# Optimization experiments

Measured on AMD Instinct MI355X. Metric: run time of the kernel, lower is better.

Reference implementation:

```python
import jax, jax.numpy as jnp
import numpy as np
import math

T, P, ITERS, H = 6, 8, 2, 8          # nr_types, num_proto, iters, n_head
D, F = 512, 1024                      # dim_proto, feature_dim (hidden_dim==D)
L = T * ITERS                         # 12 cross-attention layers


def _ln(x, g=None, b=None, eps=1e-5):
    m = x.mean(-1, keepdims=True)
    v = x.var(-1, keepdims=True)
    y = (x - m) * jax.lax.rsqrt(v + eps)
    if g is not None:
        y = y * g + b
    return y


def _forward(x_batch, batch_mask, node_type, pm_W, pm_b, pm_g, pm_bn,
             proto_logsigma, rand_mul, Wq, bq, Wk, bk, Wv, bv, Wo, bo,
             ag, ab, Wm1, bm1, lg, lb, Wm2, bm2, pg, pb):
    B, N, _ = x_batch.shape
    dt = x_batch.dtype
    bm = batch_mask.astype(dt)                                   # [B,N]
    onehot = jax.nn.one_hot(node_type, T, dtype=dt)              # [B,N,T]
    valid = bm * jnp.any(x_batch != 0, axis=-1).astype(dt)       # [B,N]
    mbt = onehot * valid[:, :, None]                             # [B,N,T]
    sums = jnp.einsum('bnt,bnf->btf', mbt, x_batch)              # per-(batch,type) sum
    cnt = mbt.sum(1)                                             # [B,T]
    fallback = x_batch.sum(1) / bm.sum(1, keepdims=True)         # [B,F]
    proto_mu = jnp.where(cnt[..., None] > 0,
                         sums / jnp.maximum(cnt, 1.0)[..., None],
                         fallback[:, None, :])                   # [B,T,F]

    # proto_mlp: Linear + LayerNorm + GELU (dropout = eval/identity)
    mu = jax.nn.gelu(_ln(proto_mu @ pm_W + pm_b, pm_g, pm_bn), approximate=False)  # [B,T,D]
    all_proto = mu[:, :, None, :] + jnp.exp(proto_logsigma)[None] * rand_mul[None]  # [B,T,P,D]

    dh = D // H
    scale = 1.0 / math.sqrt(dh)
    keymask = bm[:, None, None, :] == 0                          # [B,1,1,N]

    def layer(q, i):
        resid = q                                                 # [B,P,D]
        k = _ln((x_batch @ Wk[i] + bk[i]).reshape(B, N, H, dh))   # QK-LayerNorm (no affine)
        v = (x_batch @ Wv[i] + bv[i]).reshape(B, N, H, dh)
        qh = _ln((q @ Wq[i] + bq[i]).reshape(B, P, H, dh))
        dots = jnp.einsum('bkhd,bnhd->bkhn', qh, k) * scale       # [B,P,H,N]
        dots = jnp.where(keymask, -jnp.inf, dots)
        attn = jax.nn.softmax(dots, axis=-1)
        upd = jnp.einsum('bnhd,bkhn->bkhd', v, attn).reshape(B, P, D)
        upd = upd @ Wo[i] + bo[i]
        q = resid + _ln(upd, ag[i], ab[i])
        h = jax.nn.gelu(_ln(q @ Wm1[i] + bm1[i], lg[i], lb[i]), approximate=False)
        h = h @ Wm2[i] + bm2[i]
        return q + _ln(h, pg[i], pb[i])

    outs = []
    c = 0
    for i in range(T):
        p = all_proto[:, i]
        for _ in range(ITERS):
            p = layer(p, c)
            c += 1
        outs.append(p)
    prototypes = jnp.stack(outs, axis=1)                          # [B,T,P,D]
    return prototypes, proto_mu


def setup_inputs() -> dict:
    key = jax.random.key(0)
    ks = jax.random.split(key, 40)
    B, N = 4, 4096
    sc = 0.02

    def rn(i, shape, s=sc):
        return jax.random.normal(ks[i], shape, jnp.float32) * s

    inp = {
        'x_batch': jax.random.normal(ks[0], (B, N, F), jnp.float32),
        'batch_mask': jax.random.randint(ks[1], (B, N), 0, 2, jnp.int32),
        'node_type': jax.random.randint(ks[2], (B, N), 0, T, jnp.int32),
        'pm_W': rn(3, (F, D)), 'pm_b': jnp.zeros((D,)),
        'pm_g': jnp.ones((D,)), 'pm_bn': jnp.zeros((D,)),
        'proto_logsigma': rn(4, (T, 1, D), 0.05),
        'rand_mul': jax.random.normal(ks[5], (T, P, D), jnp.float32),
        'Wq': rn(6, (L, D, D)), 'bq': jnp.zeros((L, D)),
        'Wk': rn(7, (L, F, D)), 'bk': jnp.zeros((L, D)),
        'Wv': rn(8, (L, F, D)), 'bv': jnp.zeros((L, D)),
        'Wo': rn(9, (L, D, D)), 'bo': jnp.zeros((L, D)),
        'ag': jnp.ones((L, D)), 'ab': jnp.zeros((L, D)),
        'Wm1': rn(10, (L, D, D)), 'bm1': jnp.zeros((L, D)),
        'lg': jnp.ones((L, D)), 'lb': jnp.zeros((L, D)),
        'Wm2': rn(11, (L, D, D)), 'bm2': jnp.zeros((L, D)),
        'pg': jnp.ones((L, D)), 'pb': jnp.zeros((L, D)),
    }
    return inp


def reference(x_batch, batch_mask, node_type, pm_W, pm_b, pm_g, pm_bn,
              proto_logsigma, rand_mul, Wq, bq, Wk, bk, Wv, bv, Wo, bo,
              ag, ab, Wm1, bm1, lg, lb, Wm2, bm2, pg, pb):
    return _forward(x_batch, batch_mask, node_type, pm_W, pm_b, pm_g, pm_bn,
                    proto_logsigma, rand_mul, Wq, bq, Wk, bk, Wv, bv, Wo, bo,
                    ag, ab, Wm1, bm1, lg, lb, Wm2, bm2, pg, pb)
```

## Files before the change

### kernel.cpp

```cpp
#include <hip/hip_runtime.h>
#include <hip/hip_bf16.h>
#include <stdint.h>

#define TT 6
#define PP 8
#define HH 8
#define DD 512
#define FF 1024
#define DH 64
#define NB 4
#define NN 4096
#define LL 12
#define NCH 16
#define CHK 256
#define NXB 128

typedef __attribute__((ext_vector_type(8))) short short8v;
typedef __attribute__((ext_vector_type(4))) float f32x4;
typedef __attribute__((ext_vector_type(4))) unsigned short u16x4;
typedef __attribute__((ext_vector_type(8))) unsigned short u16x8;
typedef unsigned short u16;

__device__ __forceinline__ float bf2f(u16 u){
  union { unsigned int i; float f; } x; x.i = ((unsigned int)u) << 16; return x.f;
}
__device__ __forceinline__ u16 f2bf(float f){
  union { float f; unsigned int i; } x; x.f = f;
  unsigned int r = x.i + 0x7fffu + ((x.i >> 16) & 1u);
  return (u16)(r >> 16);
}
__device__ __forceinline__ float wave_sum(float x){
  #pragma unroll
  for (int o = 32; o > 0; o >>= 1) x += __shfl_xor(x, o);
  return x;
}
__device__ __forceinline__ float ldf(const void* p, size_t i, int f32){
  float v;
  if (f32) v = ((const float*)p)[i];
  else     v = bf2f(((const u16*)p)[i]);
  return v;
}
__device__ __forceinline__ float gemv_vec(const float* __restrict__ xs,
    const void* __restrict__ W, size_t wbase, int ktot, int wf32,
    float* __restrict__ red, int tid){
  int g = tid & 63, sl = tid >> 6;
  int kpw = ktot >> 3;
  float a[8] = {0,0,0,0,0,0,0,0};
  if (wf32){
    const float* Wp = (const float*)W + wbase + (size_t)(sl*kpw)*DD + g*8;
    #pragma unroll 4
    for (int i = 0; i < kpw; ++i){
      float xv = xs[sl*kpw + i];
      f32x4 lo = *(const f32x4*)(Wp + (size_t)i*DD);
      f32x4 hi = *(const f32x4*)(Wp + (size_t)i*DD + 4);
      a[0]+=xv*lo.x; a[1]+=xv*lo.y; a[2]+=xv*lo.z; a[3]+=xv*lo.w;
      a[4]+=xv*hi.x; a[5]+=xv*hi.y; a[6]+=xv*hi.z; a[7]+=xv*hi.w;
    }
  } else {
    const u16* Wp = (const u16*)W + wbase + (size_t)(sl*kpw)*DD + g*8;
    #pragma unroll 4
    for (int i = 0; i < kpw; ++i){
      float xv = xs[sl*kpw + i];
      u16x8 w8 = *(const u16x8*)(Wp + (size_t)i*DD);
      #pragma unroll
      for (int j = 0; j < 8; ++j) a[j] += xv * bf2f(w8[j]);
    }
  }
  #pragma unroll
  for (int j = 0; j < 8; ++j) red[sl*512 + g*8 + j] = a[j];
  __syncthreads();
  float y = 0;
  #pragma unroll
  for (int s2 = 0; s2 < 8; ++s2) y += red[s2*512 + tid];
  return y;
}
__device__ __forceinline__ void glds16(const void* g, void* l){
#if __has_builtin(__builtin_amdgcn_global_load_lds)
  __builtin_amdgcn_global_load_lds(
      (const __attribute__((address_space(1))) void*)g,
      (__attribute__((address_space(3))) void*)l, 16, 0, 0);
#else
  *(u16x8*)l = *(const u16x8*)g;
#endif
}
__device__ __forceinline__ void tail_gemm8(f32x4 acc[4], const u16* __restrict__ Bp,
    const u16* As, int l15, int q4, int n0w){
  #pragma unroll
  for (int ni = 0; ni < 4; ++ni){ f32x4 z = {0,0,0,0}; acc[ni] = z; }
  #pragma unroll 2
  for (int k0 = 0; k0 < 512; k0 += 32){
    short8v bf[4], af;
    #pragma unroll
    for (int ni = 0; ni < 4; ++ni)
      bf[ni] = *(const short8v*)(Bp + (size_t)(n0w + ni*16 + l15)*DD + k0 + q4*8);
    af = *(const short8v*)(As + l15*520 + k0 + q4*8);
    #pragma unroll
    for (int ni = 0; ni < 4; ++ni)
      acc[ni] = __builtin_amdgcn_mfma_f32_16x16x32_bf16(af, bf[ni], acc[ni], 0, 0, 0);
  }
}
__device__ __forceinline__ void row_ln8(const f32x4 acc[4],
    float* red1, float* red2, int w, int l15, int q4,
    float mv[4], float rv[4]){
  float s1[4], s2[4];
  #pragma unroll
  for (int r = 0; r < 4; ++r){
    float a0=acc[0][r], a1=acc[1][r], a2=acc[2][r], a3=acc[3][r];
    s1[r] = (a0+a1)+(a2+a3);
    s2[r] = (a0*a0+a1*a1)+(a2*a2+a3*a3);
  }
  #pragma unroll
  for (int o = 1; o < 16; o <<= 1)
    #pragma unroll
    for (int r = 0; r < 4; ++r){
      s1[r] += __shfl_xor(s1[r], o);
      s2[r] += __shfl_xor(s2[r], o);
    }
  if (l15 == 0){
    #pragma unroll
    for (int r = 0; r < 4; ++r){
      int row = q4*4 + r;
      red1[row*8 + w] = s1[r];
      red2[row*8 + w] = s2[r];
    }
  }
  __syncthreads();
  #pragma unroll
  for (int r = 0; r < 4; ++r){
    int row = q4*4 + r;
    float S1 = 0, S2 = 0;
    #pragma unroll
    for (int j = 0; j < 8; ++j){ S1 += red1[row*8+j]; S2 += red2[row*8+j]; }
    float m = S1 * (1.f/DD);
    float var = S2 * (1.f/DD) - m*m;
    mv[r] = m;
    rv[r] = rsqrtf(var + 1e-5f);
  }
  __syncthreads();
}

__global__ void k_detect(const void* __restrict__ X, int* __restrict__ flag){
  int tid = threadIdx.x;
  const u16* u = (const u16*)X;
  int bad = 0;
  for (int i = tid; i < 8192; i += 256){
    int ex = (u[i] >> 7) & 0xFF;
    if (ex >= 0x90) bad = 1;
  }
  __shared__ int s;
  if (tid == 0) s = 0;
  __syncthreads();
  if (bad) s = 1;
  __syncthreads();
  if (tid == 0) *flag = s;
}

__global__ void k_cvt2(const void* __restrict__ s0, u16* __restrict__ d0, int n0q,
                       const void* __restrict__ s1, u16* __restrict__ d1,
                       const int* __restrict__ flagp){
  int f32 = *flagp;
  size_t q = (size_t)blockIdx.x*256 + threadIdx.x;
  const void* s; u16* d; size_t i;
  if (q < (size_t)n0q){ s = s0; d = d0; i = q*4; }
  else                { s = s1; d = d1; i = (q - n0q)*4; }
  if (f32){
    f32x4 v = *(const f32x4*)((const float*)s + i);
    u16x4 o; o.x=f2bf(v.x); o.y=f2bf(v.y); o.z=f2bf(v.z); o.w=f2bf(v.w);
    *(u16x4*)(d+i) = o;
  } else {
    *(u16x4*)(d+i) = *(const u16x4*)((const u16*)s + i);
  }
}

__global__ void k_xcv(const void* __restrict__ X, u16* __restrict__ Xb,
                      const int* __restrict__ bm, const int* __restrict__ ntype,
                      float* __restrict__ Pcol, float* __restrict__ Ptot,
                      float* __restrict__ cnt, float* __restrict__ bmsum,
                      const int* __restrict__ flagp){
  int f32 = *flagp;
  int b = blockIdx.y, blk = blockIdx.x;
  int n0 = blk * 32;
  int tid = threadIdx.x;
  int f0 = tid * 4;
  __shared__ int sflag[32];
  __shared__ float scnt[TT+1];
  if (tid < 32) sflag[tid] = 0;
  if (tid < TT+1) scnt[tid] = 0.f;
  __syncthreads();
  float acc[TT][4] = {};
  float tot[4] = {0,0,0,0};
  for (int i = 0; i < 32; ++i){
    int n = n0 + i;
    size_t idx = (size_t)(b*NN+n)*FF + f0;
    u16x4 xb;
    bool a;
    if (f32){
      f32x4 v = *(const f32x4*)((const float*)X + idx);
      xb.x=f2bf(v.x); xb.y=f2bf(v.y); xb.z=f2bf(v.z); xb.w=f2bf(v.w);
      a = (v.x!=0.f)||(v.y!=0.f)||(v.z!=0.f)||(v.w!=0.f);
    } else {
      xb = *(const u16x4*)((const u16*)X + idx);
      a = (bf2f(xb.x)!=0.f)||(bf2f(xb.y)!=0.f)||(bf2f(xb.z)!=0.f)||(bf2f(xb.w)!=0.f);
    }
    *(u16x4*)(Xb+idx) = xb;
    if (a) sflag[i] = 1;
    float vbm = (bm[b*NN+n] != 0) ? 1.f : 0.f;
    int ty = ntype[b*NN+n];
    #pragma unroll
    for (int j = 0; j < 4; ++j){
      float xv = bf2f(xb[j]);
      tot[j] += xv;
      float xvv = xv * vbm;
      #pragma unroll
      for (int t = 0; t < TT; ++t) acc[t][j] += (ty==t) ? xvv : 0.f;
    }
  }
  __syncthreads();
  if (tid < 32){
    int n = n0 + tid;
    if (bm[b*NN+n] != 0){
      if (sflag[tid]) atomicAdd(&scnt[ntype[b*NN+n]], 1.f);
      atomicAdd(&scnt[TT], 1.f);
    }
  }
  size_t pbase = (size_t)blk*NB + b;
  #pragma unroll
  for (int t = 0; t < TT; ++t){
    f32x4 v = {acc[t][0], acc[t][1], acc[t][2], acc[t][3]};
    *(f32x4*)&Pcol[(pbase*TT + t)*FF + f0] = v;
  }
  {
    f32x4 v = {tot[0], tot[1], tot[2], tot[3]};
    *(f32x4*)&Ptot[pbase*FF + f0] = v;
  }
  __syncthreads();
  if (tid < TT) atomicAdd(&cnt[b*TT + tid], scnt[tid]);
  if (tid == TT) atomicAdd(&bmsum[b], scnt[TT]);
}

__global__ void k_fold(const float* __restrict__ Pcol, const float* __restrict__ Ptot,
                       float* __restrict__ colsums, float* __restrict__ coltotal){
  int fb = blockIdx.x;
  int bt = blockIdx.y;
  int b = bt / TT, t = bt % TT;
  int f = fb*256 + threadIdx.x;
  float S = 0.f;
  #pragma unroll 4
  for (int blk = 0; blk < NXB; ++blk)
    S += Pcol[(((size_t)blk*NB + b)*TT + t)*FF + f];
  colsums[(size_t)bt*FF + f] = S;
  if (t == 0){
    float T = 0.f;
    #pragma unroll 4
    for (int blk = 0; blk < NXB; ++blk)
      T += Ptot[((size_t)blk*NB + b)*FF + f];
    coltotal[b*FF + f] = T;
  }
}

__global__ void k_compact(const int* __restrict__ bm, int* __restrict__ nidx,
                          int* __restrict__ cntc){
  int b = blockIdx.x, tid = threadIdx.x;
  __shared__ int csum[256];
  __shared__ int pref[257];
  int base = b*NN + tid*16;
  int f[16]; int loc = 0;
  #pragma unroll
  for (int i = 0; i < 16; ++i){ f[i] = (bm[base+i] != 0); loc += f[i]; }
  csum[tid] = loc;
  __syncthreads();
  if (tid == 0){
    pref[0] = 0;
    for (int j = 0; j < 256; ++j) pref[j+1] = pref[j] + csum[j];
  }
  __syncthreads();
  int off = b*NN + pref[tid];
  #pragma unroll
  for (int i = 0; i < 16; ++i){ if (f[i]) nidx[off++] = tid*16 + i; }
  if (tid == 0) cntc[b] = pref[256];
}

__global__ void k_wbfT(const void* __restrict__ Wq, const void* __restrict__ Wo,
                       const void* __restrict__ Wm1, const void* __restrict__ Wm2,
                       u16* __restrict__ Wt, const int* __restrict__ flagp){
  int f32 = *flagp;
  int z = blockIdx.z;
  int fam = z / LL;
  const void* src = (fam==0) ? Wq : (fam==1) ? Wo : (fam==2) ? Wm1 : Wm2;
  size_t sbase = (size_t)(z % LL) * DD * DD;
  __shared__ u16 tile[32][33];
  int d0 = blockIdx.x*32, k0 = blockIdx.y*32;
  int tx = threadIdx.x, ty = threadIdx.y;
  #pragma unroll
  for (int i = 0; i < 4; ++i){
    size_t idx = sbase + (size_t)(k0 + ty + i*8)*DD + d0 + tx;
    u16 v;
    if (f32) v = f2bf(((const float*)src)[idx]);
    else     v = ((const u16*)src)[idx];
    tile[ty + i*8][tx] = v;
  }
  __syncthreads();
  #pragma unroll
  for (int i = 0; i < 4; ++i)
    Wt[((size_t)z*DD + d0 + ty + i*8)*DD + k0 + tx] = tile[tx][ty + i*8];
}

__global__ void __launch_bounds__(512) k_mu(const float* __restrict__ colsums,
   const float* __restrict__ coltotal, const float* __restrict__ cnt,
   const float* __restrict__ bmsum,
   const void* __restrict__ pmWx, const void* __restrict__ pmb,
   const void* __restrict__ pmg, const void* __restrict__ pmbn,
   const void* __restrict__ lsig, const void* __restrict__ rmul,
   float* __restrict__ qstate, void* __restrict__ dout, int wmode,
   const int* __restrict__ flagp){
  int f32 = *flagp;
  int wf32 = wmode ? f32 : 0;
  const size_t OFFP = (size_t)NB*TT*PP*DD;
  int bt = blockIdx.x; int b = bt/TT, t = bt%TT;
  int d = threadIdx.x;
  __shared__ float xs[FF];
  __shared__ float red[4096];
  __shared__ float r1[8], r2[8];
  float cv = cnt[bt];
  float inv = 1.f / fmaxf(cv, 1.f);
  float fbinv = 1.f / bmsum[b];
  #pragma unroll
  for (int h = 0; h < 2; ++h){
    int f = d + h*512;
    float pm = (cv > 0.f) ? colsums[(size_t)bt*FF + f] * inv
                          : coltotal[b*FF + f] * fbinv;
    xs[f] = pm;
    if (f32) ((float*)dout)[OFFP + (size_t)bt*FF + f] = pm;
    else     ((u16*)dout)[OFFP + (size_t)bt*FF + f] = f2bf(pm);
  }
  __syncthreads();
  float acc = ldf(pmb, d, f32) + gemv_vec(xs, pmWx, 0, FF, wf32, red, d);
  int lane = d & 63, wid = d >> 6;
  float s1 = wave_sum(acc), s2 = wave_sum(acc*acc);
  if (lane==0){ r1[wid]=s1; r2[wid]=s2; }
  __syncthreads();
  float m=0, qq=0;
  #pragma unroll
  for (int i=0;i<8;++i){ m+=r1[i]; qq+=r2[i]; }
  m *= (1.f/DD); float var = qq*(1.f/DD) - m*m;
  float y = (acc - m) * rsqrtf(var + 1e-5f) * ldf(pmg, d, f32) + ldf(pmbn, d, f32);
  float mu = 0.5f * y * (1.f + erff(y * 0.70710678118654752f));
  #pragma unroll
  for (int p = 0; p < PP; ++p){
    float rv = ldf(rmul, (size_t)(t*PP+p)*DD + d, f32);
    float ls = ldf(lsig, (size_t)t*DD + d, f32);
    qstate[(((size_t)(b*TT+t))*PP + p)*DD + d] = mu + expf(ls) * rv;
  }
}

__global__ void k_transpose(const void* __restrict__ Wk, const void* __restrict__ Wv,
                            u16* __restrict__ TK, u16* __restrict__ TV,
                            int tlo, int s, const int* __restrict__ flagp){
  int f32 = *flagp;
  int ti = blockIdx.z >> 1, kv = blockIdx.z & 1;
  int c = 2*(tlo+ti)+s;
  size_t eoff = (size_t)c*FF*DD;
  const void* W = kv ? Wv : Wk;
  u16* T = (kv ? TV : TK) + (size_t)ti*FF*DD;
  __shared__ u16 tile[32][33];
  int n0 = blockIdx.x * 32, k0 = blockIdx.y * 32;
  int tx = threadIdx.x, ty = threadIdx.y;
  #pragma unroll
  for (int i = 0; i < 4; ++i){
    size_t idx = eoff + (size_t)(k0 + ty + i*8)*DD + n0 + tx;
    u16 v;
    if (f32) v = f2bf(((const float*)W)[idx]);
    else     v = ((const u16*)W)[idx];
    tile[ty + i*8][tx] = v;
  }
  __syncthreads();
  #pragma unroll
  for (int i = 0; i < 4; ++i)
    T[(size_t)(n0 + ty + i*8)*FF + k0 + tx] = tile[tx][ty + i*8];
}

__global__ void __launch_bounds__(512) k_kvgemm(const u16* __restrict__ Xb,
    const u16* __restrict__ TK, const u16* __restrict__ TV,
    const void* __restrict__ bk, const void* __restrict__ bv,
    u16* __restrict__ Kb, u16* __restrict__ Vb,
    const int* __restrict__ nidx, const int* __restrict__ cntc,
    int tlo, int s, int nt, const int* __restrict__ flagp){
  int f32 = *flagp;
  int orig = blockIdx.x;
  int x = orig & 7, r = orig >> 3;
  int bx = r / nt, pr = r - bx*nt;
  int pairg = x*nt + pr;
  int by = pairg & 3; int kvti = pairg >> 2; int kv = kvti & 1; int ti = kvti >> 1;
  int b = bx >> 4, jt = bx & 15;
  int cnt = cntc[b];
  if (jt*256 >= cnt) return;
  int c = 2*(tlo+ti)+s;
  size_t boff = (size_t)c*DD;
  const u16* WT = (kv ? TV : TK) + (size_t)ti*FF*DD;
  const void* bias = kv ? bv : bk;
  u16* out = (kv ? Vb : Kb) + (size_t)ti*((size_t)NB*NN*DD);
  int n0 = by*128;
  __shared__ __align__(16) char LDS[3*24576];
  int tid = threadIdx.x, wid = tid >> 6, lane = tid & 63;
  int wr = wid >> 1, wcn = wid & 1;
  const u16* gp0; const u16* gp1; const u16* gp2;
  int lo0, lo1, lo2;
  {
    const u16* gps[3]; int los[3];
    #pragma unroll
    for (int i = 0; i < 3; ++i){
      int e = tid + i*512;
      if (e < 1024){
        int row = e>>2, sp = e&3;
        int ssrc = sp ^ (((row>>3)&1)<<1);
        int cl = jt*256 + row; if (cl >= cnt) cl = cnt-1;
        int grow = nidx[b*NN + cl];
        gps[i] = Xb + ((size_t)b*NN + grow)*FF + ssrc*8;
        los[i] = e*16;
      } else {
        int e2 = e - 1024;
        int row = e2>>2, sp = e2&3;
        int ssrc = sp ^ (((row>>3)&1)<<1);
        gps[i] = WT + (size_t)(n0 + row)*FF + ssrc*8;
        los[i] = 16384 + e2*16;
      }
    }
    gp0=gps[0]; gp1=gps[1]; gp2=gps[2];
    lo0=los[0]; lo1=los[1]; lo2=los[2];
  }
#define STAGE(T) { char* bb_ = LDS + ((T)%3)*24576; \
  glds16(gp0 + (T)*32, bb_ + lo0); glds16(gp1 + (T)*32, bb_ + lo1); \
  glds16(gp2 + (T)*32, bb_ + lo2); }
  int ke = (lane>>4) ^ (((lane>>3)&1)<<1);
  int arow[4], brow[4];
  #pragma unroll
  for (int mi = 0; mi < 4; ++mi)
    arow[mi] = (wr*64 + mi*16 + (lane&15))*64 + ke*16;
  #pragma unroll
  for (int ni = 0; ni < 4; ++ni)
    brow[ni] = 16384 + (wcn*64 + ni*16 + (lane&15))*64 + ke*16;
  f32x4 acc[4][4] = {};
  STAGE(0);
  STAGE(1);
  asm volatile("s_waitcnt vmcnt(3)" ::: "memory");
  __builtin_amdgcn_sched_barrier(0);
  __builtin_amdgcn_s_barrier();
  __builtin_amdgcn_sched_barrier(0);
  #pragma unroll
  for (int t = 0; t < 32; ++t){
    const char* Bbuf = LDS + (t%3)*24576;
    short8v af[4], bf[4];
    #pragma unroll
    for (int mi = 0; mi < 4; ++mi)
      af[mi] = *(const short8v*)(Bbuf + arow[mi]);
    #pragma unroll
    for (int ni = 0; ni < 4; ++ni)
      bf[ni] = *(const short8v*)(Bbuf + brow[ni]);
    if (t + 2 <= 31) STAGE(t+2);
    __builtin_amdgcn_s_setprio(1);
    #pragma unroll
    for (int mi = 0; mi < 4; ++mi)
      #pragma unroll
      for (int ni = 0; ni < 4; ++ni)
        acc[mi][ni] = __builtin_amdgcn_mfma_f32_16x16x32_bf16(af[mi], bf[ni], acc[mi][ni], 0, 0, 0);
    __builtin_amdgcn_s_setprio(0);
    if (t < 30)       asm volatile("s_waitcnt vmcnt(3)" ::: "memory");
    else if (t == 30) asm volatile("s_waitcnt vmcnt(0)" ::: "memory");
    __builtin_amdgcn_sched_barrier(0);
    if (t < 31){
      __builtin_amdgcn_s_barrier();
      __builtin_amdgcn_sched_barrier(0);
    }
  }
#undef STAGE
  #pragma unroll
  for (int mi = 0; mi < 4; ++mi){
    #pragma unroll
    for (int ni = 0; ni < 4; ++ni){
      int col = n0 + wcn*64 + ni*16 + (lane & 15);
      int h = col >> 6, dh = col & 63;
      float bvf = ldf(bias, boff + col, f32);
      #pragma unroll
      for (int r2 = 0; r2 < 4; ++r2){
        int row = jt*256 + wr*64 + mi*16 + (lane>>4)*4 + r2;
        out[(((size_t)(b*HH + h))*NN + row)*DH + dh] = f2bf(acc[mi][ni][r2] + bvf);
      }
    }
  }
}

__global__ void __launch_bounds__(512) k_qproj(const float* __restrict__ qstate,
      const void* __restrict__ Wq, const void* __restrict__ bq,
      float* __restrict__ qh, int tlo, int s, int wmode,
      const int* __restrict__ flagp){
  int f32 = *flagp;
  int wf32 = wmode ? f32 : 0;
  int z = blockIdx.x; int ti = z >> 5, rr = z & 31;
  int b = rr >> 3, p = rr & 7;
  int t = tlo + ti, c = 2*t + s;
  size_t woff = (size_t)c*DD*DD, boff = (size_t)c*DD;
  int d = threadIdx.x;
  __shared__ float xs[DD];
  __shared__ float red[4096];
  const float* xrow = qstate + (((size_t)(b*TT+t))*PP + p)*DD;
  xs[d] = xrow[d];
  __syncthreads();
  float acc = ldf(bq, boff + d, f32) + gemv_vec(xs, Wq, woff, DD, wf32, red, d);
  float s1 = wave_sum(acc) * (1.f/DH);
  float s2 = wave_sum(acc*acc) * (1.f/DH);
  float var = s2 - s1*s1;
  qh[(size_t)z*DD + d] = (acc - s1) * rsqrtf(var + 1e-5f);
}

__global__ void __launch_bounds__(512) k_attnA(const u16* __restrict__ Kb,
     const u16* __restrict__ Vb, const float* __restrict__ qh,
     const int* __restrict__ cntc, float* __restrict__ Opart, float* __restrict__ lpart){
  int ic = blockIdx.x, bh = blockIdx.y, ti = blockIdx.z;
  int b = bh >> 3, h = bh & 7;
  int cnt = cntc[b];
  if (ic*CHK >= cnt) return;
  int tid = threadIdx.x, p8 = tid >> 6, ln = tid & 63;
  int r8 = ln >> 3, g = ln & 7;
  __shared__ __align__(16) char KV[32768];
  __shared__ float qs[PP*DH];
  __shared__ float qsum[PP];
  __shared__ float e_lds[CHK*9];
  int rem = cnt - ic*CHK;
  float qv = qh[((size_t)(ti*32 + b*PP + p8))*DD + h*DH + ln];
  size_t tioff = (size_t)ti*((size_t)NB*NN*DD);
  const u16* Kbase = Kb + tioff + ((size_t)(b*HH + h)*NN + (size_t)ic*CHK)*DH;
  const u16* Vbase = Vb + tioff + ((size_t)(b*HH + h)*NN + (size_t)ic*CHK)*DH;
  #pragma unroll
  for (int i = 0; i < 4; ++i){
    int e = tid + i*512;
    int row = e >> 3, sp = e & 7;
    int ss = sp ^ (row & 7);
    int rr = row < rem ? row : rem-1;
    glds16(Vbase + (size_t)rr*DH + ss*8, (char*)KV + e*16);
  }
  qs[p8*DH + ln] = qv;
  {
    float sQ = wave_sum(qv);
    if (ln == 0) qsum[p8] = sQ;
  }
  asm volatile("s_waitcnt lgkmcnt(0)" ::: "memory");
  __builtin_amdgcn_sched_barrier(0);
  __builtin_amdgcn_s_barrier();
  __builtin_amdgcn_sched_barrier(0);
  #pragma unroll
  for (int it = 0; it < CHK/64; ++it){
    int nl = it*64 + p8*8 + r8;
    int rr8 = nl < rem ? nl : rem-1;
    u16x8 kv8 = *(const u16x8*)(Kbase + (size_t)rr8*DH + g*8);
    float kf[8];
    #pragma unroll
    for (int e = 0; e < 8; ++e) kf[e] = bf2f(kv8[e]);
    float sm = 0, sq = 0;
    #pragma unroll
    for (int e = 0; e < 8; ++e){ sm += kf[e]; sq += kf[e]*kf[e]; }
    #pragma unroll
    for (int o = 1; o < 8; o <<= 1){
      sm += __shfl_xor(sm, o);
      sq += __shfl_xor(sq, o);
    }
    sm *= (1.f/DH); sq = sq*(1.f/DH) - sm*sm;
    float inv = rsqrtf(sq + 1e-5f);
    float ap[8];
    #pragma unroll
    for (int p = 0; p < 8; ++p){
      f32x4 qa = *(const f32x4*)&qs[p*DH + g*8];
      f32x4 qb = *(const f32x4*)&qs[p*DH + g*8 + 4];
      ap[p] = kf[0]*qa.x + kf[1]*qa.y + kf[2]*qa.z + kf[3]*qa.w
            + kf[4]*qb.x + kf[5]*qb.y + kf[6]*qb.z + kf[7]*qb.w;
    }
    #pragma unroll
    for (int o = 1; o < 8; o <<= 1){
      #pragma unroll
      for (int p = 0; p < 8; ++p) ap[p] += __shfl_xor(ap[p], o);
    }
    float dg = (g==0)?ap[0]:(g==1)?ap[1]:(g==2)?ap[2]:(g==3)?ap[3]
             : (g==4)?ap[4]:(g==5)?ap[5]:(g==6)?ap[6]:ap[7];
    float sv = (dg - sm*qsum[g]) * inv * 0.125f;
    e_lds[nl*9 + g] = (nl < rem) ? __expf(sv) : 0.f;
  }
  __syncthreads();
  {
    float lp = 0;
    #pragma unroll
    for (int j = 0; j < CHK/64; ++j) lp += e_lds[(ln + j*64)*9 + p8];
    lp = wave_sum(lp);
    if (ln == 0) lpart[((size_t)(ti*32+bh)*NCH + ic)*PP + p8] = lp;
  }
  {
    float a0=0,a1=0,a2=0,a3=0,a4=0,a5=0,a6=0,a7=0;
    int vseg = (r8 ^ g) * 16;
    #pragma unroll 4
    for (int m = 0; m < CHK/8; ++m){
      float e = e_lds[(g + m*8)*9 + p8];
      u16x8 vv = *(const u16x8*)((const char*)KV + (g + m*8)*128 + vseg);
      a0 += e*bf2f(vv[0]); a1 += e*bf2f(vv[1]);
      a2 += e*bf2f(vv[2]); a3 += e*bf2f(vv[3]);
      a4 += e*bf2f(vv[4]); a5 += e*bf2f(vv[5]);
      a6 += e*bf2f(vv[6]); a7 += e*bf2f(vv[7]);
    }
    #pragma unroll
    for (int o = 1; o < 8; o <<= 1){
      a0 += __shfl_xor(a0, o); a1 += __shfl_xor(a1, o);
      a2 += __shfl_xor(a2, o); a3 += __shfl_xor(a3, o);
      a4 += __shfl_xor(a4, o); a5 += __shfl_xor(a5, o);
      a6 += __shfl_xor(a6, o); a7 += __shfl_xor(a7, o);
    }
    if (g == 0){
      float* op = Opart + ((size_t)(ti*32+bh)*NCH + ic)*512 + p8*64 + r8*8;
      f32x4 lo = {a0,a1,a2,a3}, hi = {a4,a5,a6,a7};
      *(f32x4*)op = lo;
      *((f32x4*)op + 1) = hi;
    }
  }
}

__global__ void __launch_bounds__(512) k_tailm(
    const float* __restrict__ Opart, const float* __restrict__ lpart,
    const int* __restrict__ cntc,
    float* __restrict__ qstate, float* __restrict__ qh,
    const u16* __restrict__ Wt,
    const void* __restrict__ bo, const void* __restrict__ ag, const void* __restrict__ ab,
    const void* __restrict__ bm1, const void* __restrict__ lg, const void* __restrict__ lb,
    const void* __restrict__ bm2, const void* __restrict__ pg, const void* __restrict__ pb,
    const void* __restrict__ bq, void* __restrict__ dout,
    int tlo, int s, int nt, const int* __restrict__ flagp){
  int f32 = *flagp;
  int ti = blockIdx.x & 7, b = blockIdx.x >> 3;
  if (ti >= nt) return;
  int t = tlo + ti, c = 2*t + s;
  int tid = threadIdx.x;
  int w = tid >> 6, lane = tid & 63, q4 = lane >> 4, l15 = lane & 15;
  int n0w = w*64;
  size_t boff = (size_t)c*DD;
  const size_t famSz = (size_t)LL*DD*DD;
  __shared__ u16 As[16*520];
  __shared__ float red1[128], red2[128];
  __shared__ float lval[64];
  int nch = (cntc[b] + CHK - 1) / CHK;
  for (int i = tid; i < 16*520; i += 512) As[i] = 0;
  if (tid < 64){
    int p = tid >> 3, hh = tid & 7;
    float l = 0;
    for (int ic = 0; ic < nch; ++ic)
      l += lpart[((size_t)(ti*32 + b*8 + hh)*NCH + ic)*PP + p];
    lval[tid] = 1.f / l;
  }
  __syncthreads();
  {
    int hh = tid >> 6, dd = tid & 63;
    #pragma unroll
    for (int p = 0; p < 8; ++p){
      float o = 0;
      for (int ic = 0; ic < nch; ++ic)
        o += Opart[((size_t)(ti*32 + b*8 + hh)*NCH + ic)*512 + p*64 + dd];
      As[p*520 + hh*64 + dd] = f2bf(o * lval[p*8 + hh]);
    }
  }
  __syncthreads();
  f32x4 acc[4], q2[4];
  float mv[4], rv[4];
  size_t qoffb = ((size_t)(b*TT+t))*PP*DD;
  {
    const u16* Bp = Wt + famSz + (size_t)c*DD*DD;
    tail_gemm8(acc, Bp, As, l15, q4, n0w);
    #pragma unroll
    for (int ni = 0; ni < 4; ++ni){
      float bv = ldf(bo, boff + n0w + ni*16 + l15, f32);
      #pragma unroll
      for (int r = 0; r < 4; ++r) acc[ni][r] += bv;
    }
    row_ln8(acc, red1, red2, w, l15, q4, mv, rv);
    #pragma unroll
    for (int ni = 0; ni < 4; ++ni){
      int col = n0w + ni*16 + l15;
      float gm = ldf(ag, boff + col, f32), bt = ldf(ab, boff + col, f32);
      #pragma unroll
      for (int r = 0; r < 4; ++r){
        int row = q4*4 + r;
        float y = (acc[ni][r] - mv[r])*rv[r]*gm + bt;
        float res = (q4 < 2) ? qstate[qoffb + (size_t)row*DD + col] : 0.f;
        q2[ni][r] = res + y;
      }
    }
    if (q4 < 2){
      #pragma unroll
      for (int r = 0; r < 4; ++r){
        int row = q4*4 + r;
        #pragma unroll
        for (int ni = 0; ni < 4; ++ni)
          As[row*520 + n0w + ni*16 + l15] = f2bf(q2[ni][r]);
      }
    }
  }
  __syncthreads();
  {
    const u16* Bp = Wt + 2*famSz + (size_t)c*DD*DD;
    tail_gemm8(acc, Bp, As, l15, q4, n0w);
    #pragma unroll
    for (int ni = 0; ni < 4; ++ni){
      float bv = ldf(bm1, boff + n0w + ni*16 + l15, f32);
      #pragma unroll
      for (int r = 0; r < 4; ++r) acc[ni][r] += bv;
    }
    row_ln8(acc, red1, red2, w, l15, q4, mv, rv);
    #pragma unroll
    for (int ni = 0; ni < 4; ++ni){
      int col = n0w + ni*16 + l15;
      float gm = ldf(lg, boff + col, f32), bt = ldf(lb, boff + col, f32);
      #pragma unroll
      for (int r = 0; r < 4; ++r){
        int row = q4*4 + r;
        float y = (acc[ni][r] - mv[r])*rv[r]*gm + bt;
        y = 0.5f*y*(1.f + erff(y*0.70710678118654752f));
        if (q4 < 2) As[row*520 + col] = f2bf(y);
      }
    }
  }
  __syncthreads();
  {
    const u16* Bp = Wt + 3*famSz + (size_t)c*DD*DD;
    tail_gemm8(acc, Bp, As, l15, q4, n0w);
    #pragma unroll
    for (int ni = 0; ni < 4; ++ni){
      float bv = ldf(bm2, boff + n0w + ni*16 + l15, f32);
      #pragma unroll
      for (int r = 0; r < 4; ++r) acc[ni][r] += bv;
    }
    row_ln8(acc, red1, red2, w, l15, q4, mv, rv);
    #pragma unroll
    for (int ni = 0; ni < 4; ++ni){
      int col = n0w + ni*16 + l15;
      float gm = ldf(pg, boff + col, f32), bt = ldf(pb, boff + col, f32);
      #pragma unroll
      for (int r = 0; r < 4; ++r){
        int row = q4*4 + r;
        float outv = q2[ni][r] + (acc[ni][r] - mv[r])*rv[r]*gm + bt;
        if (q4 < 2){
          qstate[qoffb + (size_t)row*DD + col] = outv;
          if (s == 0) As[row*520 + col] = f2bf(outv);
          else {
            if (f32) ((float*)dout)[qoffb + (size_t)row*DD + col] = outv;
            else     ((u16*)dout)[qoffb + (size_t)row*DD + col] = f2bf(outv);
          }
        }
      }
    }
  }
  if (s == 0){
    __syncthreads();
    const u16* Bp = Wt + (size_t)(c+1)*DD*DD;
    tail_gemm8(acc, Bp, As, l15, q4, n0w);
    #pragma unroll
    for (int ni = 0; ni < 4; ++ni){
      float bv = ldf(bq, (size_t)(c+1)*DD + n0w + ni*16 + l15, f32);
      #pragma unroll
      for (int r = 0; r < 4; ++r) acc[ni][r] += bv;
    }
    float s1[4], s2[4];
    #pragma unroll
    for (int r = 0; r < 4; ++r){
      float a0=acc[0][r], a1=acc[1][r], a2=acc[2][r], a3=acc[3][r];
      s1[r] = (a0+a1)+(a2+a3);
      s2[r] = (a0*a0+a1*a1)+(a2*a2+a3*a3);
    }
    #pragma unroll
    for (int o = 1; o < 16; o <<= 1)
      #pragma unroll
      for (int r = 0; r < 4; ++r){
        s1[r] += __shfl_xor(s1[r], o);
        s2[r] += __shfl_xor(s2[r], o);
      }
    if (q4 < 2){
      #pragma unroll
      for (int r = 0; r < 4; ++r){
        int row = q4*4 + r;
        float m = s1[r] * (1.f/DH);
        float var = s2[r] * (1.f/DH) - m*m;
        float ri = rsqrtf(var + 1e-5f);
        #pragma unroll
        for (int ni = 0; ni < 4; ++ni){
          int col = n0w + ni*16 + l15;
          qh[((size_t)(ti*32 + b*8 + row))*DD + col] = (acc[ni][r] - m)*ri;
        }
      }
    }
  }
}

__global__ void __launch_bounds__(512) k_tail(
    const float* __restrict__ Opart, const float* __restrict__ lpart,
    const int* __restrict__ cntc,
    float* __restrict__ qstate, float* __restrict__ qh,
    const void* __restrict__ Wo_, const void* __restrict__ Wm1_,
    const void* __restrict__ Wm2_, const void* __restrict__ Wq_,
    const void* __restrict__ bo, const void* __restrict__ ag, const void* __restrict__ ab,
    const void* __restrict__ bm1, const void* __restrict__ lg, const void* __restrict__ lb,
    const void* __restrict__ bm2, const void* __restrict__ pg, const void* __restrict__ pb,
    const void* __restrict__ bq,
    int tlo, int s, int wmode, const int* __restrict__ flagp){
  int f32 = *flagp;
  int wf32 = wmode ? f32 : 0;
  int z = blockIdx.x; int ti = z >> 5, rr = z & 31;
  int b = rr >> 3, p = rr & 7;
  int t = tlo + ti, c = 2*t + s;
  int d = threadIdx.x;
  int h = d >> 6, dd = d & 63;
  int lane = d & 63, wid = d >> 6;
  size_t qoff = (((size_t)(b*TT+t))*PP + p)*DD;
  size_t boff = (size_t)c*DD;
  size_t w0 = (size_t)c*DD*DD;
  __shared__ float xs[DD];
  __shared__ float red[4096];
  __shared__ float r1[8], r2[8];
  int nch = (cntc[b] + CHK - 1) / CHK;
  float o = 0, l = 0;
  for (int ic = 0; ic < nch; ++ic){
    o += Opart[((size_t)(ti*32 + b*8 + h)*NCH + ic)*512 + p*64 + dd];
    l += lpart[((size_t)(ti*32 + b*8 + h)*NCH + ic)*PP + p];
  }
  float upd = o / l;
  xs[d] = upd;
  __syncthreads();
  float acc = ldf(bo, boff + d, f32) + gemv_vec(xs, Wo_, w0, DD, wf32, red, d);
  {
    float s1 = wave_sum(acc), s2 = wave_sum(acc*acc);
    if (lane == 0){ r1[wid] = s1; r2[wid] = s2; }
  }
  __syncthreads();
  float m = 0, qv = 0;
  #pragma unroll
  for (int i = 0; i < 8; ++i){ m += r1[i]; qv += r2[i]; }
  m *= (1.f/DD); float var = qv*(1.f/DD) - m*m;
  float y = (acc - m)*rsqrtf(var + 1e-5f)*ldf(ag, boff+d, f32) + ldf(ab, boff+d, f32);
  float q2 = qstate[qoff + d] + y;
  __syncthreads();
  xs[d] = q2;
  __syncthreads();
  float acc2 = ldf(bm1, boff + d, f32) + gemv_vec(xs, Wm1_, w0, DD, wf32, red, d);
  {
    float s1 = wave_sum(acc2), s2 = wave_sum(acc2*acc2);
    if (lane == 0){ r1[wid] = s1; r2[wid] = s2; }
  }
  __syncthreads();
  m = 0; qv = 0;
  #pragma unroll
  for (int i = 0; i < 8; ++i){ m += r1[i]; qv += r2[i]; }
  m *= (1.f/DD); var = qv*(1.f/DD) - m*m;
  float y2 = (acc2 - m)*rsqrtf(var + 1e-5f)*ldf(lg, boff+d, f32) + ldf(lb, boff+d, f32);
  y2 = 0.5f*y2*(1.f + erff(y2*0.70710678118654752f));
  __syncthreads();
  xs[d] = y2;
  __syncthreads();
  float acc3 = ldf(bm2, boff + d, f32) + gemv_vec(xs, Wm2_, w0, DD, wf32, red, d);
  {
    float s1 = wave_sum(acc3), s2 = wave_sum(acc3*acc3);
    if (lane == 0){ r1[wid] = s1; r2[wid] = s2; }
  }
  __syncthreads();
  m = 0; qv = 0;
  #pragma unroll
  for (int i = 0; i < 8; ++i){ m += r1[i]; qv += r2[i]; }
  m *= (1.f/DD); var = qv*(1.f/DD) - m*m;
  float y3 = (acc3 - m)*rsqrtf(var + 1e-5f)*ldf(pg, boff+d, f32) + ldf(pb, boff+d, f32);
  float outv = q2 + y3;
  qstate[qoff + d] = outv;
  if (s == 0){
    __syncthreads();
    xs[d] = outv;
    __syncthreads();
    size_t w1 = (size_t)(c+1)*DD*DD;
    float accq = ldf(bq, (size_t)(c+1)*DD + d, f32) + gemv_vec(xs, Wq_, w1, DD, wf32, red, d);
    float t1 = wave_sum(accq) * (1.f/DH);
    float t2 = wave_sum(accq*accq) * (1.f/DH);
    float var2 = t2 - t1*t1;
    qh[(size_t)z*DD + d] = (accq - t1) * rsqrtf(var2 + 1e-5f);
  }
}

__global__ void k_out(const float* __restrict__ qstate, void* __restrict__ dout,
                      const int* __restrict__ flagp){
  int f32 = *flagp;
  int i = blockIdx.x*256 + threadIdx.x;
  if (f32) ((float*)dout)[i] = qstate[i];
  else     ((u16*)dout)[i] = f2bf(qstate[i]);
}

extern "C" void kernel_launch(void* const* d_in, const int* in_sizes, int n_in,
                              void* d_out, int out_size, void* d_ws, size_t ws_size,
                              hipStream_t stream){
  (void)in_sizes; (void)n_in; (void)out_size;
  const void* X   = d_in[0];
  const int* bm    = (const int*)d_in[1];
  const int* ntype = (const int*)d_in[2];
  const void* pmW = d_in[3];  const void* pmb = d_in[4];
  const void* pmg = d_in[5];  const void* pmbn= d_in[6];
  const void* lsig= d_in[7];  const void* rmul= d_in[8];
  const void* Wq  = d_in[9];  const void* bq  = d_in[10];
  const void* Wk  = d_in[11]; const void* bk  = d_in[12];
  const void* Wv  = d_in[13]; const void* bv  = d_in[14];
  const void* Wo  = d_in[15]; const void* bo  = d_in[16];
  const void* ag  = d_in[17]; const void* ab  = d_in[18];
  const void* Wm1 = d_in[19]; const void* bm1 = d_in[20];
  const void* lg  = d_in[21]; const void* lb  = d_in[22];
  const void* Wm2 = d_in[23]; const void* bm2 = d_in[24];
  const void* pg  = d_in[25]; const void* pb  = d_in[26];

  char* ws = (char*)d_ws;
  int*   flagp    = (int*)(ws + 0);
  float* cnt      = (float*)(ws + 256);
  float* bmsum    = (float*)(ws + 512);
  float* colsums  = (float*)(ws + 768);
  float* coltotal = (float*)(ws + 99072);
  float* qstate   = (float*)(ws + 279296);
  int*   cntc     = (int*)(ws + 672512);
  int*   nidx     = (int*)(ws + 672768);

  size_t off = 738304;
  auto take = [&](size_t bytes)->char*{
    char* p = ws + off; off = (off + bytes + 255) & ~(size_t)255; return p;
  };
  u16* Xbf = (u16*)take((size_t)NB*NN*FF*2);

  const size_t perT = (size_t)65536
                    + 16384
                    + 1048576
                    + 2*1048576
                    + 2*16777216;
  const size_t wtBytes = (size_t)4*LL*DD*DD*2;
  const size_t pmwbB   = (size_t)FF*DD*2;
  const size_t wqbB    = (size_t)LL*DD*DD*2;
  size_t base = off;

  int nt = 1;
  if      (ws_size >= base + 6*perT + 65536) nt = 6;
  else if (ws_size >= base + 3*perT + 65536) nt = 3;
  else if (ws_size >= base + 2*perT + 65536) nt = 2;

  float* qh    = (float*)take((size_t)nt*65536);
  float* lpart = (float*)take((size_t)nt*16384);
  float* Opart = (float*)take((size_t)nt*1048576);
  u16*   WkT   = (u16*)take((size_t)nt*1048576);
  u16*   WvT   = (u16*)take((size_t)nt*1048576);
  u16*   Kb    = (u16*)take((size_t)nt*16777216);
  u16*   Vb    = (u16*)take((size_t)nt*16777216);

  int useWt = (ws_size >= off + wtBytes + 65536) ? 1 : 0;
  u16* Wt = useWt ? (u16*)take(wtBytes) : nullptr;
  int useCvt = (ws_size >= off + pmwbB + wqbB + 65536) ? 1 : 0;
  u16* pmWb = useCvt ? (u16*)take(pmwbB) : nullptr;
  u16* Wqb  = useCvt ? (u16*)take(wqbB)  : nullptr;

  const void* WqG = useCvt ? (const void*)Wqb : Wq;
  int wmode = useCvt ? 0 : 1;

  float* Pcol = (float*)Kb;
  float* Ptot = (float*)((char*)Kb + (size_t)NXB*NB*TT*FF*4);

  hipMemsetAsync(ws + 256, 0, 512, stream);
  k_detect<<<1, 256, 0, stream>>>(X, flagp);
  k_compact<<<NB, 256, 0, stream>>>(bm, nidx, cntc);
  if (useWt)
    k_wbfT<<<dim3(16, 16, 4*LL), dim3(32, 8), 0, stream>>>(Wq, Wo, Wm1, Wm2, Wt, flagp);
  if (useCvt){
    const int n0q = (FF*DD)/4;
    const int nblk = (FF*DD + LL*DD*DD)/4/256;
    k_cvt2<<<nblk, 256, 0, stream>>>(pmW, pmWb, n0q, Wq, Wqb, flagp);
  }
  k_xcv<<<dim3(NXB, NB), 256, 0, stream>>>(X, Xbf, bm, ntype, Pcol, Ptot,
                                           cnt, bmsum, flagp);
  k_fold<<<dim3(4, NB*TT), 256, 0, stream>>>(Pcol, Ptot, colsums, coltotal);
  if (useCvt)
    k_mu<<<NB*TT, 512, 0, stream>>>(colsums, coltotal, cnt, bmsum,
        pmWb, pmb, pmg, pmbn, lsig, rmul, qstate, d_out, 0, flagp);
  else
    k_mu<<<NB*TT, 512, 0, stream>>>(colsums, coltotal, cnt, bmsum,
        pmW, pmb, pmg, pmbn, lsig, rmul, qstate, d_out, 1, flagp);

  for (int tlo = 0; tlo < TT; tlo += nt){
    for (int s = 0; s < 2; ++s){
      k_transpose<<<dim3(16, 32, 2*nt), dim3(32, 8), 0, stream>>>(
          Wk, Wv, WkT, WvT, tlo, s, flagp);
      k_kvgemm<<<64*8*nt, 512, 0, stream>>>(
          Xbf, WkT, WvT, bk, bv, Kb, Vb, nidx, cntc, tlo, s, nt, flagp);
      if (s == 0)
        k_qproj<<<nt*32, 512, 0, stream>>>(qstate, WqG, bq, qh, tlo, 0, wmode, flagp);
      k_attnA<<<dim3(NCH, 32, nt), 512, 0, stream>>>(Kb, Vb, qh, cntc, Opart, lpart);
      if (useWt)
        k_tailm<<<32, 512, 0, stream>>>(Opart, lpart, cntc, qstate, qh, Wt,
            bo, ag, ab, bm1, lg, lb, bm2, pg, pb, bq, d_out, tlo, s, nt, flagp);
      else
        k_tail<<<nt*32, 512, 0, stream>>>(Opart, lpart, cntc, qstate, qh,
            Wo, Wm1, Wm2, Wq, bo, ag, ab, bm1, lg, lb, bm2, pg, pb, bq,
            tlo, s, 1, flagp);
    }
  }
  if (!useWt)
    k_out<<<NB*TT*PP*DD/256, 256, 0, stream>>>(qstate, d_out, flagp);
}
```

Measured before the change: 619.0 us.

## Drop MFMA tail kernel and transposed bf16 weight prep; use per-row GEMV tail

Removes the k_wbfT pre-transposition of Wq/Wo/Wm1/Wm2 into bf16 and the k_tailm MFMA tail, which ran only 32 blocks (one per batch×type slot, batched over prototypes). Every launch now uses the per-row k_tail GEMV path over nt*32 blocks, which reads the original weights and, when the converted copy exists, the bf16 Wq. k_tail now writes the final output on the second sub-iteration, so the separate k_out kernel is no longer launched. The aim is to save the upfront weight transpose and spread the tail over more blocks. The cost is scalar GEMV work instead of matrix-core MFMA, and Wo, Wm1 and Wm2 are re-read from the original, possibly fp32, inputs.

```diff
diff --git a/kernel.cpp b/kernel.cpp
--- a/kernel.cpp
+++ b/kernel.cpp
@@ -82,61 +82,6 @@
 #else
   *(u16x8*)l = *(const u16x8*)g;
 #endif
-}
-__device__ __forceinline__ void tail_gemm8(f32x4 acc[4], const u16* __restrict__ Bp,
-    const u16* As, int l15, int q4, int n0w){
-  #pragma unroll
-  for (int ni = 0; ni < 4; ++ni){ f32x4 z = {0,0,0,0}; acc[ni] = z; }
-  #pragma unroll 2
-  for (int k0 = 0; k0 < 512; k0 += 32){
-    short8v bf[4], af;
-    #pragma unroll
-    for (int ni = 0; ni < 4; ++ni)
-      bf[ni] = *(const short8v*)(Bp + (size_t)(n0w + ni*16 + l15)*DD + k0 + q4*8);
-    af = *(const short8v*)(As + l15*520 + k0 + q4*8);
-    #pragma unroll
-    for (int ni = 0; ni < 4; ++ni)
-      acc[ni] = __builtin_amdgcn_mfma_f32_16x16x32_bf16(af, bf[ni], acc[ni], 0, 0, 0);
-  }
-}
-__device__ __forceinline__ void row_ln8(const f32x4 acc[4],
-    float* red1, float* red2, int w, int l15, int q4,
-    float mv[4], float rv[4]){
-  float s1[4], s2[4];
-  #pragma unroll
-  for (int r = 0; r < 4; ++r){
-    float a0=acc[0][r], a1=acc[1][r], a2=acc[2][r], a3=acc[3][r];
-    s1[r] = (a0+a1)+(a2+a3);
-    s2[r] = (a0*a0+a1*a1)+(a2*a2+a3*a3);
-  }
-  #pragma unroll
-  for (int o = 1; o < 16; o <<= 1)
-    #pragma unroll
-    for (int r = 0; r < 4; ++r){
-      s1[r] += __shfl_xor(s1[r], o);
-      s2[r] += __shfl_xor(s2[r], o);
-    }
-  if (l15 == 0){
-    #pragma unroll
-    for (int r = 0; r < 4; ++r){
-      int row = q4*4 + r;
-      red1[row*8 + w] = s1[r];
-      red2[row*8 + w] = s2[r];
-    }
-  }
-  __syncthreads();
-  #pragma unroll
-  for (int r = 0; r < 4; ++r){
-    int row = q4*4 + r;
-    float S1 = 0, S2 = 0;
-    #pragma unroll
-    for (int j = 0; j < 8; ++j){ S1 += red1[row*8+j]; S2 += red2[row*8+j]; }
-    float m = S1 * (1.f/DD);
-    float var = S2 * (1.f/DD) - m*m;
-    mv[r] = m;
-    rv[r] = rsqrtf(var + 1e-5f);
-  }
-  __syncthreads();
 }
 
 __global__ void k_detect(const void* __restrict__ X, int* __restrict__ flag){
@@ -278,31 +223,6 @@
   #pragma unroll
   for (int i = 0; i < 16; ++i){ if (f[i]) nidx[off++] = tid*16 + i; }
   if (tid == 0) cntc[b] = pref[256];
-}
-
-__global__ void k_wbfT(const void* __restrict__ Wq, const void* __restrict__ Wo,
-                       const void* __restrict__ Wm1, const void* __restrict__ Wm2,
-                       u16* __restrict__ Wt, const int* __restrict__ flagp){
-  int f32 = *flagp;
-  int z = blockIdx.z;
-  int fam = z / LL;
-  const void* src = (fam==0) ? Wq : (fam==1) ? Wo : (fam==2) ? Wm1 : Wm2;
-  size_t sbase = (size_t)(z % LL) * DD * DD;
-  __shared__ u16 tile[32][33];
-  int d0 = blockIdx.x*32, k0 = blockIdx.y*32;
-  int tx = threadIdx.x, ty = threadIdx.y;
-  #pragma unroll
-  for (int i = 0; i < 4; ++i){
-    size_t idx = sbase + (size_t)(k0 + ty + i*8)*DD + d0 + tx;
-    u16 v;
-    if (f32) v = f2bf(((const float*)src)[idx]);
-    else     v = ((const u16*)src)[idx];
-    tile[ty + i*8][tx] = v;
-  }
-  __syncthreads();
-  #pragma unroll
-  for (int i = 0; i < 4; ++i)
-    Wt[((size_t)z*DD + d0 + ty + i*8)*DD + k0 + tx] = tile[tx][ty + i*8];
 }
 
 __global__ void __launch_bounds__(512) k_mu(const float* __restrict__ colsums,
@@ -619,179 +539,6 @@
   }
 }
 
-__global__ void __launch_bounds__(512) k_tailm(
-    const float* __restrict__ Opart, const float* __restrict__ lpart,
-    const int* __restrict__ cntc,
-    float* __restrict__ qstate, float* __restrict__ qh,
-    const u16* __restrict__ Wt,
-    const void* __restrict__ bo, const void* __restrict__ ag, const void* __restrict__ ab,
-    const void* __restrict__ bm1, const void* __restrict__ lg, const void* __restrict__ lb,
-    const void* __restrict__ bm2, const void* __restrict__ pg, const void* __restrict__ pb,
-    const void* __restrict__ bq, void* __restrict__ dout,
-    int tlo, int s, int nt, const int* __restrict__ flagp){
-  int f32 = *flagp;
-  int ti = blockIdx.x & 7, b = blockIdx.x >> 3;
-  if (ti >= nt) return;
-  int t = tlo + ti, c = 2*t + s;
-  int tid = threadIdx.x;
-  int w = tid >> 6, lane = tid & 63, q4 = lane >> 4, l15 = lane & 15;
-  int n0w = w*64;
-  size_t boff = (size_t)c*DD;
-  const size_t famSz = (size_t)LL*DD*DD;
-  __shared__ u16 As[16*520];
-  __shared__ float red1[128], red2[128];
-  __shared__ float lval[64];
-  int nch = (cntc[b] + CHK - 1) / CHK;
-  for (int i = tid; i < 16*520; i += 512) As[i] = 0;
-  if (tid < 64){
-    int p = tid >> 3, hh = tid & 7;
-    float l = 0;
-    for (int ic = 0; ic < nch; ++ic)
-      l += lpart[((size_t)(ti*32 + b*8 + hh)*NCH + ic)*PP + p];
-    lval[tid] = 1.f / l;
-  }
-  __syncthreads();
-  {
-    int hh = tid >> 6, dd = tid & 63;
-    #pragma unroll
-    for (int p = 0; p < 8; ++p){
-      float o = 0;
-      for (int ic = 0; ic < nch; ++ic)
-        o += Opart[((size_t)(ti*32 + b*8 + hh)*NCH + ic)*512 + p*64 + dd];
-      As[p*520 + hh*64 + dd] = f2bf(o * lval[p*8 + hh]);
-    }
-  }
-  __syncthreads();
-  f32x4 acc[4], q2[4];
-  float mv[4], rv[4];
-  size_t qoffb = ((size_t)(b*TT+t))*PP*DD;
-  {
-    const u16* Bp = Wt + famSz + (size_t)c*DD*DD;
-    tail_gemm8(acc, Bp, As, l15, q4, n0w);
-    #pragma unroll
-    for (int ni = 0; ni < 4; ++ni){
-      float bv = ldf(bo, boff + n0w + ni*16 + l15, f32);
-      #pragma unroll
-      for (int r = 0; r < 4; ++r) acc[ni][r] += bv;
-    }
-    row_ln8(acc, red1, red2, w, l15, q4, mv, rv);
-    #pragma unroll
-    for (int ni = 0; ni < 4; ++ni){
-      int col = n0w + ni*16 + l15;
-      float gm = ldf(ag, boff + col, f32), bt = ldf(ab, boff + col, f32);
-      #pragma unroll
-      for (int r = 0; r < 4; ++r){
-        int row = q4*4 + r;
-        float y = (acc[ni][r] - mv[r])*rv[r]*gm + bt;
-        float res = (q4 < 2) ? qstate[qoffb + (size_t)row*DD + col] : 0.f;
-        q2[ni][r] = res + y;
-      }
-    }
-    if (q4 < 2){
-      #pragma unroll
-      for (int r = 0; r < 4; ++r){
-        int row = q4*4 + r;
-        #pragma unroll
-        for (int ni = 0; ni < 4; ++ni)
-          As[row*520 + n0w + ni*16 + l15] = f2bf(q2[ni][r]);
-      }
-    }
-  }
-  __syncthreads();
-  {
-    const u16* Bp = Wt + 2*famSz + (size_t)c*DD*DD;
-    tail_gemm8(acc, Bp, As, l15, q4, n0w);
-    #pragma unroll
-    for (int ni = 0; ni < 4; ++ni){
-      float bv = ldf(bm1, boff + n0w + ni*16 + l15, f32);
-      #pragma unroll
-      for (int r = 0; r < 4; ++r) acc[ni][r] += bv;
-    }
-    row_ln8(acc, red1, red2, w, l15, q4, mv, rv);
-    #pragma unroll
-    for (int ni = 0; ni < 4; ++ni){
-      int col = n0w + ni*16 + l15;
-      float gm = ldf(lg, boff + col, f32), bt = ldf(lb, boff + col, f32);
-      #pragma unroll
-      for (int r = 0; r < 4; ++r){
-        int row = q4*4 + r;
-        float y = (acc[ni][r] - mv[r])*rv[r]*gm + bt;
-        y = 0.5f*y*(1.f + erff(y*0.70710678118654752f));
-        if (q4 < 2) As[row*520 + col] = f2bf(y);
-      }
-    }
-  }
-  __syncthreads();
-  {
-    const u16* Bp = Wt + 3*famSz + (size_t)c*DD*DD;
-    tail_gemm8(acc, Bp, As, l15, q4, n0w);
-    #pragma unroll
-    for (int ni = 0; ni < 4; ++ni){
-      float bv = ldf(bm2, boff + n0w + ni*16 + l15, f32);
-      #pragma unroll
-      for (int r = 0; r < 4; ++r) acc[ni][r] += bv;
-    }
-    row_ln8(acc, red1, red2, w, l15, q4, mv, rv);
-    #pragma unroll
-    for (int ni = 0; ni < 4; ++ni){
-      int col = n0w + ni*16 + l15;
-      float gm = ldf(pg, boff + col, f32), bt = ldf(pb, boff + col, f32);
-      #pragma unroll
-      for (int r = 0; r < 4; ++r){
-        int row = q4*4 + r;
-        float outv = q2[ni][r] + (acc[ni][r] - mv[r])*rv[r]*gm + bt;
-        if (q4 < 2){
-          qstate[qoffb + (size_t)row*DD + col] = outv;
-          if (s == 0) As[row*520 + col] = f2bf(outv);
-          else {
-            if (f32) ((float*)dout)[qoffb + (size_t)row*DD + col] = outv;
-            else     ((u16*)dout)[qoffb + (size_t)row*DD + col] = f2bf(outv);
-          }
-        }
-      }
-    }
-  }
-  if (s == 0){
-    __syncthreads();
-    const u16* Bp = Wt + (size_t)(c+1)*DD*DD;
-    tail_gemm8(acc, Bp, As, l15, q4, n0w);
-    #pragma unroll
-    for (int ni = 0; ni < 4; ++ni){
-      float bv = ldf(bq, (size_t)(c+1)*DD + n0w + ni*16 + l15, f32);
-      #pragma unroll
-      for (int r = 0; r < 4; ++r) acc[ni][r] += bv;
-    }
-    float s1[4], s2[4];
-    #pragma unroll
-    for (int r = 0; r < 4; ++r){
-      float a0=acc[0][r], a1=acc[1][r], a2=acc[2][r], a3=acc[3][r];
-      s1[r] = (a0+a1)+(a2+a3);
-      s2[r] = (a0*a0+a1*a1)+(a2*a2+a3*a3);
-    }
-    #pragma unroll
-    for (int o = 1; o < 16; o <<= 1)
-      #pragma unroll
-      for (int r = 0; r < 4; ++r){
-        s1[r] += __shfl_xor(s1[r], o);
-        s2[r] += __shfl_xor(s2[r], o);
-      }
-    if (q4 < 2){
-      #pragma unroll
-      for (int r = 0; r < 4; ++r){
-        int row = q4*4 + r;
-        float m = s1[r] * (1.f/DH);
-        float var = s2[r] * (1.f/DH) - m*m;
-        float ri = rsqrtf(var + 1e-5f);
-        #pragma unroll
-        for (int ni = 0; ni < 4; ++ni){
-          int col = n0w + ni*16 + l15;
-          qh[((size_t)(ti*32 + b*8 + row))*DD + col] = (acc[ni][r] - m)*ri;
-        }
-      }
-    }
-  }
-}
-
 __global__ void __launch_bounds__(512) k_tail(
     const float* __restrict__ Opart, const float* __restrict__ lpart,
     const int* __restrict__ cntc,
@@ -801,8 +548,8 @@
     const void* __restrict__ bo, const void* __restrict__ ag, const void* __restrict__ ab,
     const void* __restrict__ bm1, const void* __restrict__ lg, const void* __restrict__ lb,
     const void* __restrict__ bm2, const void* __restrict__ pg, const void* __restrict__ pb,
-    const void* __restrict__ bq,
-    int tlo, int s, int wmode, const int* __restrict__ flagp){
+    const void* __restrict__ bq, void* __restrict__ dout,
+    int tlo, int s, int wmode, int wqmode, const int* __restrict__ flagp){
   int f32 = *flagp;
   int wf32 = wmode ? f32 : 0;
   int z = blockIdx.x; int ti = z >> 5, rr = z & 31;
@@ -869,25 +616,22 @@
   float y3 = (acc3 - m)*rsqrtf(var + 1e-5f)*ldf(pg, boff+d, f32) + ldf(pb, boff+d, f32);
   float outv = q2 + y3;
   qstate[qoff + d] = outv;
+  if (s == 1){
+    if (f32) ((float*)dout)[qoff + d] = outv;
+    else     ((u16*)dout)[qoff + d] = f2bf(outv);
+  }
   if (s == 0){
     __syncthreads();
     xs[d] = outv;
     __syncthreads();
     size_t w1 = (size_t)(c+1)*DD*DD;
-    float accq = ldf(bq, (size_t)(c+1)*DD + d, f32) + gemv_vec(xs, Wq_, w1, DD, wf32, red, d);
+    int wq32 = wqmode ? f32 : 0;
+    float accq = ldf(bq, (size_t)(c+1)*DD + d, f32) + gemv_vec(xs, Wq_, w1, DD, wq32, red, d);
     float t1 = wave_sum(accq) * (1.f/DH);
     float t2 = wave_sum(accq*accq) * (1.f/DH);
     float var2 = t2 - t1*t1;
     qh[(size_t)z*DD + d] = (accq - t1) * rsqrtf(var2 + 1e-5f);
   }
-}
-
-__global__ void k_out(const float* __restrict__ qstate, void* __restrict__ dout,
-                      const int* __restrict__ flagp){
-  int f32 = *flagp;
-  int i = blockIdx.x*256 + threadIdx.x;
-  if (f32) ((float*)dout)[i] = qstate[i];
-  else     ((u16*)dout)[i] = f2bf(qstate[i]);
 }
 
 extern "C" void kernel_launch(void* const* d_in, const int* in_sizes, int n_in,
@@ -931,7 +675,6 @@
                     + 1048576
                     + 2*1048576
                     + 2*16777216;
-  const size_t wtBytes = (size_t)4*LL*DD*DD*2;
   const size_t pmwbB   = (size_t)FF*DD*2;
   const size_t wqbB    = (size_t)LL*DD*DD*2;
   size_t base = off;
@@ -949,8 +692,6 @@
   u16*   Kb    = (u16*)take((size_t)nt*16777216);
   u16*   Vb    = (u16*)take((size_t)nt*16777216);
 
-  int useWt = (ws_size >= off + wtBytes + 65536) ? 1 : 0;
-  u16* Wt = useWt ? (u16*)take(wtBytes) : nullptr;
   int useCvt = (ws_size >= off + pmwbB + wqbB + 65536) ? 1 : 0;
   u16* pmWb = useCvt ? (u16*)take(pmwbB) : nullptr;
   u16* Wqb  = useCvt ? (u16*)take(wqbB)  : nullptr;
@@ -964,8 +705,6 @@
   hipMemsetAsync(ws + 256, 0, 512, stream);
   k_detect<<<1, 256, 0, stream>>>(X, flagp);
   k_compact<<<NB, 256, 0, stream>>>(bm, nidx, cntc);
-  if (useWt)
-    k_wbfT<<<dim3(16, 16, 4*LL), dim3(32, 8), 0, stream>>>(Wq, Wo, Wm1, Wm2, Wt, flagp);
   if (useCvt){
     const int n0q = (FF*DD)/4;
     const int nblk = (FF*DD + LL*DD*DD)/4/256;
@@ -990,15 +729,9 @@
       if (s == 0)
         k_qproj<<<nt*32, 512, 0, stream>>>(qstate, WqG, bq, qh, tlo, 0, wmode, flagp);
       k_attnA<<<dim3(NCH, 32, nt), 512, 0, stream>>>(Kb, Vb, qh, cntc, Opart, lpart);
-      if (useWt)
-        k_tailm<<<32, 512, 0, stream>>>(Opart, lpart, cntc, qstate, qh, Wt,
-            bo, ag, ab, bm1, lg, lb, bm2, pg, pb, bq, d_out, tlo, s, nt, flagp);
-      else
-        k_tail<<<nt*32, 512, 0, stream>>>(Opart, lpart, cntc, qstate, qh,
-            Wo, Wm1, Wm2, Wq, bo, ag, ab, bm1, lg, lb, bm2, pg, pb, bq,
-            tlo, s, 1, flagp);
-    }
-  }
-  if (!useWt)
-    k_out<<<NB*TT*PP*DD/256, 256, 0, stream>>>(qstate, d_out, flagp);
-}
+      k_tail<<<nt*32, 512, 0, stream>>>(Opart, lpart, cntc, qstate, qh,
+          Wo, Wm1, Wm2, WqG, bo, ag, ab, bm1, lg, lb, bm2, pg, pb, bq, d_out,
+          tlo, s, 1, wmode, flagp);
+    }
+  }
+}
```

Measured after the change: 616.3 us. Within noise of the previous version (-0.4%).
